# Kernel tuning notes

Hardware: AMD Instinct MI355X
Metric: run time of the kernel (lower is better)

The kernel has to match this reference:

```python
import jax, jax.numpy as jnp
import numpy as np

N = 100_000   # nodes
E = 1_600_000 # edges
F = 32        # input features
G = 512       # graphs in batch
EPS = 1e-5    # batchnorm eps


def setup_inputs() -> dict:
    key = jax.random.key(0)
    ks = jax.random.split(key, 24)
    d = {
        "x": jax.random.normal(ks[0], (N, F), jnp.float32),
        "edge_index": jax.random.randint(ks[1], (2, E), 0, N),
        "batch": jnp.sort(jax.random.randint(ks[2], (N,), 0, G)),
        "Wl1": jax.random.normal(ks[3], (30, F), jnp.float32) * 0.1,
        "bl1": jax.random.normal(ks[4], (30,), jnp.float32) * 0.1,
        "Wr1": jax.random.normal(ks[5], (30, F), jnp.float32) * 0.1,
        "Wl2": jax.random.normal(ks[6], (30, 30), jnp.float32) * 0.1,
        "bl2": jax.random.normal(ks[7], (30,), jnp.float32) * 0.1,
        "Wr2": jax.random.normal(ks[8], (30, 30), jnp.float32) * 0.1,
        "g1": jax.random.uniform(ks[9], (30,), jnp.float32) + 0.5,
        "b1": jax.random.normal(ks[10], (30,), jnp.float32) * 0.1,
        "m1": jax.random.normal(ks[11], (30,), jnp.float32) * 0.1,
        "v1": jax.random.uniform(ks[12], (30,), jnp.float32) + 0.5,
        "g2": jax.random.uniform(ks[13], (30,), jnp.float32) + 0.5,
        "b2": jax.random.normal(ks[14], (30,), jnp.float32) * 0.1,
        "m2": jax.random.normal(ks[15], (30,), jnp.float32) * 0.1,
        "v2": jax.random.uniform(ks[16], (30,), jnp.float32) + 0.5,
        "W1": jax.random.normal(ks[17], (10, 60), jnp.float32) * 0.1,
        "bb1": jax.random.normal(ks[18], (10,), jnp.float32) * 0.1,
        "W2": jax.random.normal(ks[19], (1, 10), jnp.float32) * 0.1,
        "bb2": jax.random.normal(ks[20], (1,), jnp.float32) * 0.1,
    }
    return d


def reference(x, edge_index, batch, Wl1, bl1, Wr1, Wl2, bl2, Wr2,
              g1, b1, m1, v1, g2, b2, m2, v2, W1, bb1, W2, bb2):
    src, dst = edge_index[0], edge_index[1]

    def sage(h, Wl, bl, Wr):
        # mean aggregation of source features into targets (PyG SAGEConv default)
        s = jax.ops.segment_sum(h[src], dst, num_segments=N)
        cnt = jax.ops.segment_sum(jnp.ones((E,), h.dtype), dst, num_segments=N)
        agg = s / jnp.maximum(cnt, 1.0)[:, None]
        return agg @ Wl.T + bl + h @ Wr.T

    def bn(h, g, b, m, v):  # BatchNorm1d, eval mode (running stats)
        return (h - m) * jax.lax.rsqrt(v + EPS) * g + b

    h = bn(jax.nn.relu(sage(x, Wl1, bl1, Wr1)), g1, b1, m1, v1)
    h = bn(jax.nn.relu(sage(h, Wl2, bl2, Wr2)), g2, b2, m2, v2)

    # dual segment pooling over graphs
    xmax = jax.ops.segment_max(h, batch, num_segments=G)
    xmax = jnp.where(jnp.isfinite(xmax), xmax, 0.0)  # empty graphs -> 0
    s = jax.ops.segment_sum(h, batch, num_segments=G)
    c = jax.ops.segment_sum(jnp.ones((N,), h.dtype), batch, num_segments=G)
    xmean = s / jnp.maximum(c, 1.0)[:, None]

    z = jnp.concatenate([xmax, xmean], axis=1)  # [G, 60]
    z = jax.nn.relu(z @ W1.T + bb1)
    z = z @ W2.T + bb2
    return jax.nn.sigmoid(z)  # [G, 1]
```

## Files before the change

kernel.cpp:

```cpp
#include <hip/hip_runtime.h>
#include <hip/hip_fp16.h>

#define NN 100000
#define NE 1600000
#define FI 32
#define FH 30
#define PAD 32
#define NG 512
#define NBK 782
#define BNODES 128
#define SCB 2048
#define CBLK 32
#define NCHUNK (SCB / CBLK)
#define CAP 4096
#define NB1 391

__global__ __launch_bounds__(256) void k_phist(const int* __restrict__ dst, int* __restrict__ partial)
{
    __shared__ int cnt[NBK];
    for (int i = threadIdx.x; i < NBK; i += 256) cnt[i] = 0;
    __syncthreads();
    for (int e = blockIdx.x * 256 + threadIdx.x; e < NE; e += SCB * 256)
        atomicAdd(&cnt[dst[e] >> 7], 1);
    __syncthreads();
    for (int i = threadIdx.x; i < NBK; i += 256)
        partial[(size_t)blockIdx.x * NBK + i] = cnt[i];
}

__global__ __launch_bounds__(256) void k_csum(const int* __restrict__ partial, int* __restrict__ chunksum)
{
    int t = blockIdx.x * 256 + threadIdx.x;
    if (t >= NCHUNK * NBK) return;
    int c = t / NBK, b = t - c * NBK;
    int s = 0;
    #pragma unroll 8
    for (int k = 0; k < CBLK; ++k)
        s += partial[(size_t)(c * CBLK + k) * NBK + b];
    chunksum[c * NBK + b] = s;
}

__global__ __launch_bounds__(1024) void k_cscan(const int* __restrict__ chunksum,
                                                int* __restrict__ chunkbase, int* __restrict__ bktOff)
{
    __shared__ int tmp[1024];
    int tid = threadIdx.x;
    int total = 0;
    if (tid < NBK) {
        for (int c = 0; c < NCHUNK; ++c) total += chunksum[c * NBK + tid];
    }
    tmp[tid] = (tid < NBK) ? total : 0;
    __syncthreads();
    for (int off = 1; off < 1024; off <<= 1) {
        int t = (tid >= off) ? tmp[tid - off] : 0;
        __syncthreads();
        tmp[tid] += t;
        __syncthreads();
    }
    if (tid < NBK) {
        int run = tmp[tid] - total;
        bktOff[tid] = run;
        for (int c = 0; c < NCHUNK; ++c) {
            chunkbase[c * NBK + tid] = run;
            run += chunksum[c * NBK + tid];
        }
    }
    if (tid == 0) bktOff[NBK] = NE;
}

__global__ __launch_bounds__(256) void k_base(int* __restrict__ partial, const int* __restrict__ chunkbase)
{
    int t = blockIdx.x * 256 + threadIdx.x;
    if (t >= NCHUNK * NBK) return;
    int c = t / NBK, b = t - c * NBK;
    int run = chunkbase[c * NBK + b];
    #pragma unroll 8
    for (int k = 0; k < CBLK; ++k) {
        size_t idx = (size_t)(c * CBLK + k) * NBK + b;
        int v = partial[idx];
        partial[idx] = run;
        run += v;
    }
}

__global__ __launch_bounds__(256) void k_bscat(const int* __restrict__ src, const int* __restrict__ dst,
                                               const int* __restrict__ partial, unsigned* __restrict__ pairs)
{
    __shared__ int sbase[NBK];
    __shared__ int scnt[NBK];
    for (int i = threadIdx.x; i < NBK; i += 256) {
        sbase[i] = partial[(size_t)blockIdx.x * NBK + i];
        scnt[i] = 0;
    }
    __syncthreads();
    for (int e = blockIdx.x * 256 + threadIdx.x; e < NE; e += SCB * 256) {
        int d = dst[e];
        int b = d >> 7;
        int r = atomicAdd(&scnt[b], 1);
        pairs[sbase[b] + r] = ((unsigned)src[e] << 7) | (unsigned)(d & 127);
    }
}

__global__ __launch_bounds__(256) void k_csr(
    const int* __restrict__ bktOff, const unsigned* __restrict__ pairs,
    int* __restrict__ rowstart, int* __restrict__ col)
{
    __shared__ unsigned sp[CAP];
    __shared__ int bins[BNODES], binpos[BNODES], stmp[BNODES];
    int tid = threadIdx.x;
    int bkt = blockIdx.x;
    int gbase = bktOff[bkt];
    int cnt = bktOff[bkt + 1] - gbase;
    if (tid < BNODES) bins[tid] = 0;
    __syncthreads();
    bool inl = (cnt <= CAP);
    if (inl) {
        for (int i = tid; i < cnt; i += 256) {
            unsigned u = pairs[gbase + i];
            sp[i] = u;
            atomicAdd(&bins[u & 127], 1);
        }
    } else {
        for (int i = tid; i < cnt; i += 256)
            atomicAdd(&bins[pairs[gbase + i] & 127], 1);
    }
    __syncthreads();
    if (tid < BNODES) stmp[tid] = bins[tid];
    __syncthreads();
    for (int off = 1; off < BNODES; off <<= 1) {
        int t = 0;
        if (tid < BNODES && tid >= off) t = stmp[tid - off];
        __syncthreads();
        if (tid < BNODES) stmp[tid] += t;
        __syncthreads();
    }
    if (tid < BNODES) {
        int ex = stmp[tid] - bins[tid];
        binpos[tid] = ex;
        int n = (bkt << 7) + tid;
        if (n < NN) rowstart[n] = gbase + ex;
        if (bkt == 0 && tid == 0) rowstart[NN] = NE;
    }
    __syncthreads();
    if (inl) {
        for (int i = tid; i < cnt; i += 256) {
            unsigned u = sp[i];
            int p = atomicAdd(&binpos[u & 127], 1);
            col[gbase + p] = (int)(u >> 7);
        }
    } else {
        for (int i = tid; i < cnt; i += 256) {
            unsigned u = pairs[gbase + i];
            int p = atomicAdd(&binpos[u & 127], 1);
            col[gbase + p] = (int)(u >> 7);
        }
    }
}

__global__ __launch_bounds__(256) void k_tohalf(const float* __restrict__ in, __half2* __restrict__ outp)
{
    int i = blockIdx.x * 256 + threadIdx.x;
    if (i < NN * (PAD / 2)) {
        float2 f = ((const float2*)in)[i];
        outp[i] = __floats2half2_rn(f.x, f.y);
    }
}

__global__ __launch_bounds__(256) void k_aggcsr_h(const int* __restrict__ rowstart,
                                                  const int* __restrict__ col,
                                                  const uint4* __restrict__ hin,
                                                  float* __restrict__ aggout)
{
    int tid = blockIdx.x * 256 + threadIdx.x;
    int n = tid >> 6;
    if (n >= NN) return;
    int lane = threadIdx.x & 63;
    int q = lane & 3;
    int grp = lane >> 2;
    int rs = rowstart[n], re = rowstart[n + 1];
    float a0 = 0.0f, a1 = 0.0f, a2 = 0.0f, a3 = 0.0f;
    float a4 = 0.0f, a5 = 0.0f, a6 = 0.0f, a7 = 0.0f;
    for (int e = rs + grp; e < re; e += 16) {
        uint4 u = hin[(size_t)col[e] * 4 + q];
        float2 f0 = __half22float2(*(const __half2*)&u.x);
        float2 f1 = __half22float2(*(const __half2*)&u.y);
        float2 f2 = __half22float2(*(const __half2*)&u.z);
        float2 f3 = __half22float2(*(const __half2*)&u.w);
        a0 += f0.x; a1 += f0.y; a2 += f1.x; a3 += f1.y;
        a4 += f2.x; a5 += f2.y; a6 += f3.x; a7 += f3.y;
    }
    #pragma unroll
    for (int off = 4; off < 64; off <<= 1) {
        a0 += __shfl_xor(a0, off); a1 += __shfl_xor(a1, off);
        a2 += __shfl_xor(a2, off); a3 += __shfl_xor(a3, off);
        a4 += __shfl_xor(a4, off); a5 += __shfl_xor(a5, off);
        a6 += __shfl_xor(a6, off); a7 += __shfl_xor(a7, off);
    }
    if (lane < 4) {
        float inv = (re > rs) ? 1.0f / (float)(re - rs) : 0.0f;
        float4* o = (float4*)(aggout + (size_t)n * PAD + q * 8);
        o[0] = make_float4(a0 * inv, a1 * inv, a2 * inv, a3 * inv);
        o[1] = make_float4(a4 * inv, a5 * inv, a6 * inv, a7 * inv);
    }
}

__global__ __launch_bounds__(256) void k_t1(
    const float* __restrict__ x, const float* __restrict__ agg,
    const float* __restrict__ Wl, const float* __restrict__ bl, const float* __restrict__ Wr,
    const float* __restrict__ g, const float* __restrict__ b,
    const float* __restrict__ m, const float* __restrict__ v,
    __half2* __restrict__ h1h)
{
    __shared__ float sWl[FH * FI], sWr[FH * FI], sBias[FH], sScale[FH], sShift[FH];
    for (int i = threadIdx.x; i < FH * FI; i += 256) { sWl[i] = Wl[i]; sWr[i] = Wr[i]; }
    if (threadIdx.x < FH) {
        int j = threadIdx.x;
        float sc = g[j] * rsqrtf(v[j] + 1e-5f);
        sBias[j] = bl[j];
        sScale[j] = sc;
        sShift[j] = b[j] - m[j] * sc;
    }
    __syncthreads();
    int n = blockIdx.x * 256 + threadIdx.x;
    if (n >= NN) return;
    float xr[FI], ar[FI];
    #pragma unroll
    for (int k = 0; k < FI; k += 4) {
        float4 xv = *(const float4*)(x + (size_t)n * FI + k);
        float4 av = *(const float4*)(agg + (size_t)n * PAD + k);
        xr[k] = xv.x; xr[k+1] = xv.y; xr[k+2] = xv.z; xr[k+3] = xv.w;
        ar[k] = av.x; ar[k+1] = av.y; ar[k+2] = av.z; ar[k+3] = av.w;
    }
    float res[FH];
    for (int j = 0; j < FH; ++j) {
        float acc = sBias[j];
        #pragma unroll
        for (int k = 0; k < FI; ++k)
            acc += ar[k] * sWl[j * FI + k] + xr[k] * sWr[j * FI + k];
        acc = fmaxf(acc, 0.0f);
        res[j] = acc * sScale[j] + sShift[j];
    }
    __half2* row = h1h + (size_t)n * (PAD / 2);
    #pragma unroll
    for (int j = 0; j < FH; j += 2)
        row[j >> 1] = __floats2half2_rn(res[j], res[j + 1]);
    row[15] = __floats2half2_rn(0.0f, 0.0f);
}

__global__ __launch_bounds__(256) void k_t2(
    const __half2* __restrict__ h1h, const float* agg,
    const float* __restrict__ Wl, const float* __restrict__ bl, const float* __restrict__ Wr,
    const float* __restrict__ g, const float* __restrict__ b,
    const float* __restrict__ m, const float* __restrict__ v,
    float* hout)
{
    __shared__ float sWl[FH * FH], sWr[FH * FH], sBias[FH], sScale[FH], sShift[FH];
    for (int i = threadIdx.x; i < FH * FH; i += 256) { sWl[i] = Wl[i]; sWr[i] = Wr[i]; }
    if (threadIdx.x < FH) {
        int j = threadIdx.x;
        float sc = g[j] * rsqrtf(v[j] + 1e-5f);
        sBias[j] = bl[j];
        sScale[j] = sc;
        sShift[j] = b[j] - m[j] * sc;
    }
    __syncthreads();
    int n = blockIdx.x * 256 + threadIdx.x;
    if (n >= NN) return;
    float xr[FH], ar[FH];
    const __half2* hrow = h1h + (size_t)n * (PAD / 2);
    #pragma unroll
    for (int k2 = 0; k2 < FH / 2; ++k2) {
        float2 fv = __half22float2(hrow[k2]);
        xr[2 * k2] = fv.x; xr[2 * k2 + 1] = fv.y;
    }
    #pragma unroll
    for (int k = 0; k < FH; ++k)
        ar[k] = agg[(size_t)n * PAD + k];
    float res[FH];
    for (int j = 0; j < FH; ++j) {
        float acc = sBias[j];
        #pragma unroll
        for (int k = 0; k < FH; ++k)
            acc += ar[k] * sWl[j * FH + k] + xr[k] * sWr[j * FH + k];
        acc = fmaxf(acc, 0.0f);
        res[j] = acc * sScale[j] + sShift[j];
    }
    #pragma unroll
    for (int j = 0; j < FH; ++j)
        hout[(size_t)n * PAD + j] = res[j];
}

__global__ __launch_bounds__(256) void k_pool(
    const float* __restrict__ h2, const int* __restrict__ batch,
    const float* __restrict__ W1, const float* __restrict__ bb1,
    const float* __restrict__ W2, const float* __restrict__ bb2,
    float* __restrict__ out)
{
    __shared__ float sS[8][FH], sM[8][FH], sz[2 * FH], st[10];
    int tid = threadIdx.x;
    int gi = blockIdx.x;
    int lo = 0, hi = NN;
    while (lo < hi) { int mid = (lo + hi) >> 1; if (batch[mid] < gi) lo = mid + 1; else hi = mid; }
    int start = lo;
    hi = NN;
    while (lo < hi) { int mid = (lo + hi) >> 1; if (batch[mid] <= gi) lo = mid + 1; else hi = mid; }
    int end = lo;

    int f = tid & 31;
    int ng = tid >> 5;
    float sum = 0.0f, mx = -INFINITY;
    if (f < FH) {
        for (int n = start + ng; n < end; n += 8) {
            float val = h2[(size_t)n * PAD + f];
            sum += val;
            mx = fmaxf(mx, val);
        }
        sS[ng][f] = sum;
        sM[ng][f] = mx;
    }
    __syncthreads();
    if (tid < FH) {
        float s = 0.0f, mm = -INFINITY;
        #pragma unroll
        for (int w = 0; w < 8; ++w) { s += sS[w][tid]; mm = fmaxf(mm, sM[w][tid]); }
        int c = end - start;
        sz[tid]      = (c > 0) ? mm : 0.0f;
        sz[FH + tid] = (c > 0) ? s / (float)c : 0.0f;
    }
    __syncthreads();
    if (tid < 10) {
        float t = bb1[tid];
        for (int k = 0; k < 2 * FH; ++k) t += sz[k] * W1[tid * 2 * FH + k];
        st[tid] = fmaxf(t, 0.0f);
    }
    __syncthreads();
    if (tid == 0) {
        float o = bb2[0];
        for (int j = 0; j < 10; ++j) o += st[j] * W2[j];
        out[gi] = 1.0f / (1.0f + expf(-o));
    }
}

extern "C" void kernel_launch(void* const* d_in, const int* in_sizes, int n_in,
                              void* d_out, int out_size, void* d_ws, size_t ws_size,
                              hipStream_t stream)
{
    const float* x   = (const float*)d_in[0];
    const int*   ei  = (const int*)d_in[1];
    const int*   bat = (const int*)d_in[2];
    const float* Wl1 = (const float*)d_in[3];
    const float* bl1 = (const float*)d_in[4];
    const float* Wr1 = (const float*)d_in[5];
    const float* Wl2 = (const float*)d_in[6];
    const float* bl2 = (const float*)d_in[7];
    const float* Wr2 = (const float*)d_in[8];
    const float* g1  = (const float*)d_in[9];
    const float* b1  = (const float*)d_in[10];
    const float* m1  = (const float*)d_in[11];
    const float* v1  = (const float*)d_in[12];
    const float* g2  = (const float*)d_in[13];
    const float* b2  = (const float*)d_in[14];
    const float* m2  = (const float*)d_in[15];
    const float* v2  = (const float*)d_in[16];
    const float* W1  = (const float*)d_in[17];
    const float* bb1 = (const float*)d_in[18];
    const float* W2  = (const float*)d_in[19];
    const float* bb2 = (const float*)d_in[20];

    const int* src = ei;
    const int* dst = ei + NE;

    int* wsi = (int*)d_ws;
    int*      partial   = wsi;
    int*      chunksum  = partial + (size_t)SCB * NBK;
    int*      chunkbase = chunksum + NCHUNK * NBK;
    int*      bktOff    = chunkbase + NCHUNK * NBK;
    int*      rowstart  = bktOff + NBK + 2;
    unsigned* pairs     = (unsigned*)(rowstart + NN + 4);
    int*      col       = (int*)(pairs + NE);
    __half2*  xh        = (__half2*)(col + NE);
    __half2*  h1h       = xh + (size_t)NN * (PAD / 2);
    float*    aggbuf    = (float*)(h1h + (size_t)NN * (PAD / 2));

    int pb = (NCHUNK * NBK + 255) / 256;

    k_phist <<<SCB, 256, 0, stream>>>(dst, partial);
    k_tohalf<<<(NN * (PAD / 2) + 255) / 256, 256, 0, stream>>>(x, (__half2*)xh);
    k_csum  <<<pb, 256, 0, stream>>>(partial, chunksum);
    k_cscan <<<1, 1024, 0, stream>>>(chunksum, chunkbase, bktOff);
    k_base  <<<pb, 256, 0, stream>>>(partial, chunkbase);
    k_bscat <<<SCB, 256, 0, stream>>>(src, dst, partial, pairs);
    k_csr   <<<NBK, 256, 0, stream>>>(bktOff, pairs, rowstart, col);

    int ab = (NN * 64 + 255) / 256;
    k_aggcsr_h<<<ab, 256, 0, stream>>>(rowstart, col, (const uint4*)xh, aggbuf);
    k_t1<<<NB1, 256, 0, stream>>>(x, aggbuf, Wl1, bl1, Wr1, g1, b1, m1, v1, h1h);
    k_aggcsr_h<<<ab, 256, 0, stream>>>(rowstart, col, (const uint4*)h1h, aggbuf);
    k_t2<<<NB1, 256, 0, stream>>>(h1h, aggbuf, Wl2, bl2, Wr2, g2, b2, m2, v2, aggbuf);
    k_pool<<<NG, 256, 0, stream>>>(aggbuf, bat, W1, bb1, W2, bb2, (float*)d_out);
}
```

Baseline: 202.2 us.

## Fuse half conversion into histogram, halve scan blocks, store layer-2 output as fp16

The fp32-to-fp16 conversion of x now runs as extra blocks of the histogram kernel, which removes one launch. The number of histogram and scatter blocks is halved, which shrinks the partial-count arrays that the chunk-sum and base kernels read and write. The chunk scan keeps its per-chunk sums in registers instead of reading them twice from global memory. The second SAGE layer now writes its output as fp16, which halves the bytes the pooling kernel reads, at the cost of reduced precision in the pooled values.

```diff
diff --git a/kernel.cpp b/kernel.cpp
--- a/kernel.cpp
+++ b/kernel.cpp
@@ -9,15 +9,25 @@
 #define NG 512
 #define NBK 782
 #define BNODES 128
-#define SCB 2048
+#define SCB 1024
 #define CBLK 32
 #define NCHUNK (SCB / CBLK)
 #define CAP 4096
 #define NB1 391
-
-__global__ __launch_bounds__(256) void k_phist(const int* __restrict__ dst, int* __restrict__ partial)
+#define THB 6250
+
+__global__ __launch_bounds__(256) void k_phist(const int* __restrict__ dst, int* __restrict__ partial,
+                                               const float* __restrict__ x, __half2* __restrict__ xh)
 {
     __shared__ int cnt[NBK];
+    if (blockIdx.x >= SCB) {
+        int i = (blockIdx.x - SCB) * 256 + threadIdx.x;
+        if (i < NN * (PAD / 2)) {
+            float2 f = ((const float2*)x)[i];
+            xh[i] = __floats2half2_rn(f.x, f.y);
+        }
+        return;
+    }
     for (int i = threadIdx.x; i < NBK; i += 256) cnt[i] = 0;
     __syncthreads();
     for (int e = blockIdx.x * 256 + threadIdx.x; e < NE; e += SCB * 256)
@@ -44,9 +54,11 @@
 {
     __shared__ int tmp[1024];
     int tid = threadIdx.x;
+    int cs[NCHUNK];
     int total = 0;
     if (tid < NBK) {
-        for (int c = 0; c < NCHUNK; ++c) total += chunksum[c * NBK + tid];
+        #pragma unroll
+        for (int c = 0; c < NCHUNK; ++c) { cs[c] = chunksum[c * NBK + tid]; total += cs[c]; }
     }
     tmp[tid] = (tid < NBK) ? total : 0;
     __syncthreads();
@@ -59,10 +71,8 @@
     if (tid < NBK) {
         int run = tmp[tid] - total;
         bktOff[tid] = run;
-        for (int c = 0; c < NCHUNK; ++c) {
-            chunkbase[c * NBK + tid] = run;
-            run += chunksum[c * NBK + tid];
-        }
+        #pragma unroll
+        for (int c = 0; c < NCHUNK; ++c) { chunkbase[c * NBK + tid] = run; run += cs[c]; }
     }
     if (tid == 0) bktOff[NBK] = NE;
 }
@@ -153,15 +163,6 @@
             int p = atomicAdd(&binpos[u & 127], 1);
             col[gbase + p] = (int)(u >> 7);
         }
-    }
-}
-
-__global__ __launch_bounds__(256) void k_tohalf(const float* __restrict__ in, __half2* __restrict__ outp)
-{
-    int i = blockIdx.x * 256 + threadIdx.x;
-    if (i < NN * (PAD / 2)) {
-        float2 f = ((const float2*)in)[i];
-        outp[i] = __floats2half2_rn(f.x, f.y);
     }
 }
 
@@ -247,11 +248,11 @@
 }
 
 __global__ __launch_bounds__(256) void k_t2(
-    const __half2* __restrict__ h1h, const float* agg,
+    const __half2* __restrict__ h1h, const float* __restrict__ agg,
     const float* __restrict__ Wl, const float* __restrict__ bl, const float* __restrict__ Wr,
     const float* __restrict__ g, const float* __restrict__ b,
     const float* __restrict__ m, const float* __restrict__ v,
-    float* hout)
+    __half2* __restrict__ h2h)
 {
     __shared__ float sWl[FH * FH], sWr[FH * FH], sBias[FH], sScale[FH], sShift[FH];
     for (int i = threadIdx.x; i < FH * FH; i += 256) { sWl[i] = Wl[i]; sWr[i] = Wr[i]; }
@@ -284,13 +285,15 @@
         acc = fmaxf(acc, 0.0f);
         res[j] = acc * sScale[j] + sShift[j];
     }
-    #pragma unroll
-    for (int j = 0; j < FH; ++j)
-        hout[(size_t)n * PAD + j] = res[j];
+    __half2* row = h2h + (size_t)n * (PAD / 2);
+    #pragma unroll
+    for (int j = 0; j < FH; j += 2)
+        row[j >> 1] = __floats2half2_rn(res[j], res[j + 1]);
+    row[15] = __floats2half2_rn(0.0f, 0.0f);
 }
 
 __global__ __launch_bounds__(256) void k_pool(
-    const float* __restrict__ h2, const int* __restrict__ batch,
+    const __half* __restrict__ h2, const int* __restrict__ batch,
     const float* __restrict__ W1, const float* __restrict__ bb1,
     const float* __restrict__ W2, const float* __restrict__ bb2,
     float* __restrict__ out)
@@ -310,7 +313,7 @@
     float sum = 0.0f, mx = -INFINITY;
     if (f < FH) {
         for (int n = start + ng; n < end; n += 8) {
-            float val = h2[(size_t)n * PAD + f];
+            float val = __half2float(h2[(size_t)n * PAD + f]);
             sum += val;
             mx = fmaxf(mx, val);
         }
@@ -379,12 +382,12 @@
     int*      col       = (int*)(pairs + NE);
     __half2*  xh        = (__half2*)(col + NE);
     __half2*  h1h       = xh + (size_t)NN * (PAD / 2);
-    float*    aggbuf    = (float*)(h1h + (size_t)NN * (PAD / 2));
+    __half2*  h2h       = h1h + (size_t)NN * (PAD / 2);
+    float*    aggbuf    = (float*)(h2h + (size_t)NN * (PAD / 2));
 
     int pb = (NCHUNK * NBK + 255) / 256;
 
-    k_phist <<<SCB, 256, 0, stream>>>(dst, partial);
-    k_tohalf<<<(NN * (PAD / 2) + 255) / 256, 256, 0, stream>>>(x, (__half2*)xh);
+    k_phist <<<SCB + THB, 256, 0, stream>>>(dst, partial, x, xh);
     k_csum  <<<pb, 256, 0, stream>>>(partial, chunksum);
     k_cscan <<<1, 1024, 0, stream>>>(chunksum, chunkbase, bktOff);
     k_base  <<<pb, 256, 0, stream>>>(partial, chunkbase);
@@ -395,6 +398,6 @@
     k_aggcsr_h<<<ab, 256, 0, stream>>>(rowstart, col, (const uint4*)xh, aggbuf);
     k_t1<<<NB1, 256, 0, stream>>>(x, aggbuf, Wl1, bl1, Wr1, g1, b1, m1, v1, h1h);
     k_aggcsr_h<<<ab, 256, 0, stream>>>(rowstart, col, (const uint4*)h1h, aggbuf);
-    k_t2<<<NB1, 256, 0, stream>>>(h1h, aggbuf, Wl2, bl2, Wr2, g2, b2, m2, v2, aggbuf);
-    k_pool<<<NG, 256, 0, stream>>>(aggbuf, bat, W1, bb1, W2, bb2, (float*)d_out);
-}
+    k_t2<<<NB1, 256, 0, stream>>>(h1h, aggbuf, Wl2, bl2, Wr2, g2, b2, m2, v2, h2h);
+    k_pool<<<NG, 256, 0, stream>>>((const __half*)h2h, bat, W1, bb1, W2, bb2, (float*)d_out);
+}
```

Result: faster. 193.4 us (-4.3%).
